# Kernel tuning notes

Hardware: AMD Instinct MI355X
Metric: run time of the kernel (lower is better)

The kernel has to match this reference:

```python
import jax, jax.numpy as jnp
import numpy as np

EPS_NORM = 1e-7
EPS_FLOW = 1e-8
GAMMA = 5.0
ETA = 1.0
NU = 1.0
SIGMA = 0.1
TAU_FLOW, TAU_COLOR, TAU_PROX = 0.8, 0.7, 0.5
SAM_TEMP = 1.0  # sam_weight used as temperature


def _cdist(x):
    # x: [B,N,D] -> pairwise euclidean distances [B,N,N]
    sq = jnp.sum(x * x, axis=-1)
    d2 = sq[..., :, None] + sq[..., None, :] - 2.0 * jnp.einsum('bnd,bmd->bnm', x, x)
    return jnp.sqrt(jnp.maximum(d2, 0.0))


def _within_sample_loss(features, sim_scores, tau, mask):
    # features: [B,N,D] (raw), sim_scores: [B,N,N], mask: [B,N] float
    nf = features / (jnp.linalg.norm(features, axis=-1, keepdims=True) + EPS_NORM)
    g_plus = jax.nn.sigmoid(-GAMMA * (tau - sim_scores))   # 1/(1+exp(gamma*(tau-s)))
    g_minus = jax.nn.sigmoid(-GAMMA * (sim_scores - tau))  # 1/(1+exp(gamma*(s-tau)))
    fs = jnp.einsum('bnd,bmd->bnm', nf, nf)
    s_plus_exp = jnp.sum(jnp.exp(ETA * fs * g_plus), axis=-1)   # [B,N]
    s_minus_exp = jnp.sum(jnp.exp(-NU * fs * g_minus), axis=-1)
    loss_per_point = jnp.log1p(s_plus_exp) / ETA + jnp.log1p(s_minus_exp) / NU
    loss_per_point = loss_per_point * mask
    valid_points = jnp.sum(mask, axis=-1)
    loss = jnp.mean(jnp.sum(loss_per_point, axis=-1) / valid_points)
    return -loss


def _sam_loss(features, labels):
    # masked_contrastive_loss with temperature = sam_weight
    nf = features / (jnp.linalg.norm(features, axis=-1, keepdims=True) + EPS_NORM)
    logits = jnp.einsum('bnd,bmd->bnm', nf, nf) / SAM_TEMP
    pos = (labels[:, :, None] == labels[:, None, :]).astype(logits.dtype)
    neg = 1.0 - pos
    exp_logits = jnp.exp(logits)
    denom = exp_logits + jnp.sum(exp_logits * neg, axis=2, keepdims=True)
    neg_log_likelihood = -jnp.log(exp_logits / denom)
    w = pos / jnp.maximum(jnp.sum(pos, axis=2, keepdims=True), 1e-6)
    nll = jnp.sum(neg_log_likelihood * w, axis=2)  # [B,N]
    pos_sum = jnp.sum(pos, axis=2)
    valid = 1.0 - (pos_sum == 0).astype(logits.dtype)
    w2 = valid / jnp.maximum(jnp.sum(valid, axis=1, keepdims=True), 1e-6)
    return jnp.mean(jnp.sum(nll * w2, axis=1))


def _forward(features, flow, points, colors_f, mask_f, sam):
    m_outer = mask_f[:, :, None] * mask_f[:, None, :]
    # flow cosine similarity
    fn = jnp.linalg.norm(flow, axis=-1)
    flow_sim = jnp.einsum('bnd,bmd->bnm', flow, flow) / (fn[:, :, None] * fn[:, None, :] + EPS_FLOW)
    flow_sim = flow_sim * m_outer
    # color similarity: 1 - normalized euclidean distance of RGB/255
    c = colors_f / 255.0
    color_sim = (1.0 - _cdist(c) / jnp.sqrt(jnp.asarray(c.shape[-1], c.dtype))) * m_outer
    # proximity similarity
    prox_sim = jnp.exp(-_cdist(points) / (2.0 * SIGMA ** 2)) * m_outer

    flow_loss = _within_sample_loss(features, flow_sim, TAU_FLOW, mask_f)
    color_loss = _within_sample_loss(features, color_sim, TAU_COLOR, mask_f)
    prox_loss = _within_sample_loss(features, prox_sim, TAU_PROX, mask_f)
    sam_loss = _sam_loss(features, sam)
    return 1.0 * flow_loss + 1.0 * color_loss + 1.0 * prox_loss + 1.0 * sam_loss


def setup_inputs() -> dict:
    key = jax.random.key(0)
    k1, k2, k3, k4, k5 = jax.random.split(key, 5)
    B, N, D = 4, 2048, 64
    features = jax.random.normal(k1, (B, N, D), dtype=jnp.float32)
    flow = jax.random.normal(k2, (B, N, 3), dtype=jnp.float32)
    points = jax.random.uniform(k3, (B, N, 3), dtype=jnp.float32)
    colors = jax.random.randint(k4, (B, N, 3), 0, 256, dtype=jnp.int32)
    sam = jax.random.randint(k5, (B, N), 0, 64, dtype=jnp.int32)
    mask = jnp.ones((B, N), dtype=bool)
    return {"features": features, "flow": flow, "points": points,
            "colors": colors, "sam": sam, "mask": mask}


def reference(features, flow, points, colors, sam, mask):
    mask_f = mask.astype(features.dtype)
    colors_f = colors.astype(features.dtype)
    return _forward(features, flow, points, colors_f, mask_f, sam)
```

## Files before the change

kernel.cpp:

```cpp
#include <hip/hip_runtime.h>

typedef unsigned short ushort_t;
typedef unsigned int uint_t;
typedef __attribute__((ext_vector_type(8))) short short8;
typedef __attribute__((ext_vector_type(4))) float float4v;

#define NPTS 2048
#define DIM 64
#define BATCH 4
#define CH 16
#define MC 128
#define NFS 72

__device__ inline float fexp2(float x){ return __builtin_amdgcn_exp2f(x); }
__device__ inline float frcp(float x){ return __builtin_amdgcn_rcpf(x); }
__device__ inline float fsqrt_(float x){ return __builtin_amdgcn_sqrtf(x); }

__device__ inline ushort_t f2bf(float x){
    uint_t u = __float_as_uint(x);
    u += 0x7FFF + ((u >> 16) & 1);
    return (ushort_t)(u >> 16);
}

__global__ __launch_bounds__(256) void fpc_prep(
    const float* __restrict__ feat, const float* __restrict__ flow,
    const float* __restrict__ pts, const int* __restrict__ cols,
    ushort_t* __restrict__ nf_g, float* __restrict__ aux_g)
{
    int t = blockIdx.x * 256 + threadIdx.x;
    const float4* f4 = (const float4*)(feat + (size_t)t * DIM);
    float v[DIM];
    float ss = 0.f;
#pragma unroll
    for (int i = 0; i < 16; i++){
        float4 x = f4[i];
        v[4*i+0] = x.x; v[4*i+1] = x.y; v[4*i+2] = x.z; v[4*i+3] = x.w;
        ss += x.x*x.x + x.y*x.y + x.z*x.z + x.w*x.w;
    }
    float inv = frcp(fsqrt_(ss) + 1e-7f);
    uint_t* np_ = (uint_t*)(nf_g + (size_t)t * DIM);
#pragma unroll
    for (int i = 0; i < 32; i++){
        uint_t lo = f2bf(v[2*i] * inv), hi = f2bf(v[2*i+1] * inv);
        np_[i] = lo | (hi << 16);
    }
    float fx = flow[t*3+0], fy = flow[t*3+1], fz = flow[t*3+2];
    float fa = fsqrt_(fx*fx + fy*fy + fz*fz);
    float* a = aux_g + (size_t)t * 10;
    a[0]=fx; a[1]=fy; a[2]=fz; a[3]=fa;
    a[4]=pts[t*3+0]; a[5]=pts[t*3+1]; a[6]=pts[t*3+2];
    const float s255 = 1.0f/255.0f;
    a[7]=(float)cols[t*3+0]*s255; a[8]=(float)cols[t*3+1]*s255; a[9]=(float)cols[t*3+2]*s255;
}

__global__ __launch_bounds__(256) void fpc_main(
    const ushort_t* __restrict__ nf_g, const float* __restrict__ aux_g,
    const int* __restrict__ lab_g, float* __restrict__ part)
{
    __shared__ __align__(16) ushort_t lds_nf[MC * NFS];
    __shared__ float lds_aux[MC * 10];
    __shared__ int lds_lab[MC];

    const int tid = threadIdx.x;
    const int ch = blockIdx.x, rg = blockIdx.y, b = blockIdx.z;
    const int mbase = ch * MC;
    const int bpt = b * NPTS;

#pragma unroll
    for (int i = 0; i < 4; i++){
        int cid = tid + i * 256;
        int row = cid >> 3, sub = cid & 7;
        const uint4* src = (const uint4*)(nf_g + (size_t)(bpt + mbase + row) * DIM + sub * 8);
        *(uint4*)(&lds_nf[row * NFS + sub * 8]) = *src;
    }
    {
        const float* asrc = aux_g + (size_t)(bpt + mbase) * 10;
#pragma unroll
        for (int i = 0; i < 5; i++){ int w = tid + i * 256; lds_aux[w] = asrc[w]; }
        if (tid < MC) lds_lab[tid] = lab_g[bpt + mbase + tid];
    }
    __syncthreads();

    const int lane = tid & 63, wave = tid >> 6;
    const int q = lane >> 4, c = lane & 15;
    const int rowA = rg * 64 + wave * 16;

    const ushort_t* arow = nf_g + (size_t)(bpt + rowA + c) * DIM;
    short8 a0 = *(const short8*)(arow + q * 8);
    short8 a1 = *(const short8*)(arow + 32 + q * 8);

    float rf[4][10]; int rlab[4];
#pragma unroll
    for (int r = 0; r < 4; r++){
        int n = bpt + rowA + q * 4 + r;
        const float* a = aux_g + (size_t)n * 10;
#pragma unroll
        for (int k = 0; k < 10; k++) rf[r][k] = a[k];
        rlab[r] = lab_g[n];
    }

    float acc[4][10];
#pragma unroll
    for (int r = 0; r < 4; r++)
#pragma unroll
        for (int k = 0; k < 10; k++) acc[r][k] = 0.0f;

    const float L2E  = 1.4426950408889634f;
    const float GL2E = 7.213475204444817f;
    const float CF = GL2E * 0.8f, CC = GL2E * 0.7f, CP = GL2E * 0.5f;

    for (int mt = 0; mt < MC / 16; mt++){
        int mloc = mt * 16 + c;
        const ushort_t* brow = &lds_nf[mloc * NFS];
        short8 b0 = *(const short8*)(brow + q * 8);
        short8 b1 = *(const short8*)(brow + 32 + q * 8);
        float4v fs4 = {0.f, 0.f, 0.f, 0.f};
        fs4 = __builtin_amdgcn_mfma_f32_16x16x32_bf16(a0, b0, fs4, 0, 0, 0);
        fs4 = __builtin_amdgcn_mfma_f32_16x16x32_bf16(a1, b1, fs4, 0, 0, 0);

        const float* ma = &lds_aux[mloc * 10];
        float m0=ma[0], m1=ma[1], m2=ma[2], m3=ma[3], m4=ma[4];
        float m5=ma[5], m6=ma[6], m7=ma[7], m8=ma[8], m9=ma[9];
        int mlab = lds_lab[mloc];

#pragma unroll
        for (int r = 0; r < 4; r++){
            float fs = fs4[r];
            float efs = L2E * fs;
            float dotf = rf[r][0]*m0 + rf[r][1]*m1 + rf[r][2]*m2;
            float sflow = dotf * frcp(rf[r][3]*m3 + 1e-8f);
            {
                float u  = fexp2(CF - GL2E * sflow);
                float gp = frcp(1.0f + u);
                float gm = 1.0f - gp;
                acc[r][0] += fexp2(efs * gp);
                acc[r][1] += fexp2(-efs * gm);
            }
            float dx = rf[r][7]-m7, dy = rf[r][8]-m8, dz = rf[r][9]-m9;
            float scol = 1.0f - fsqrt_(dx*dx + dy*dy + dz*dz) * 0.5773502691896258f;
            {
                float u  = fexp2(CC - GL2E * scol);
                float gp = frcp(1.0f + u);
                float gm = 1.0f - gp;
                acc[r][2] += fexp2(efs * gp);
                acc[r][3] += fexp2(-efs * gm);
            }
            float px = rf[r][4]-m4, py = rf[r][5]-m5, pz = rf[r][6]-m6;
            float dpt = fsqrt_(px*px + py*py + pz*pz);
            float sprox = fexp2(dpt * -72.13475204444817f);
            {
                float u  = fexp2(CP - GL2E * sprox);
                float gp = frcp(1.0f + u);
                float gm = 1.0f - gp;
                acc[r][4] += fexp2(efs * gp);
                acc[r][5] += fexp2(-efs * gm);
            }
            float e = fexp2(efs);
            acc[r][6] += e;
            bool pos = (rlab[r] == mlab);
            acc[r][7] += pos ? e : 0.0f;
            acc[r][8] += pos ? fs : 0.0f;
            acc[r][9] += pos ? 1.0f : 0.0f;
        }
    }

#pragma unroll
    for (int r = 0; r < 4; r++)
#pragma unroll
        for (int k = 0; k < 10; k++){
            float v = acc[r][k];
            v += __shfl_xor(v, 1, 64);
            v += __shfl_xor(v, 2, 64);
            v += __shfl_xor(v, 4, 64);
            v += __shfl_xor(v, 8, 64);
            acc[r][k] = v;
        }
    if (c == 0){
#pragma unroll
        for (int r = 0; r < 4; r++){
            int n = rowA + q * 4 + r;
            size_t base = ((size_t)(b * CH + ch) * 10) * NPTS + n;
#pragma unroll
            for (int k = 0; k < 10; k++) part[base + (size_t)k * NPTS] = acc[r][k];
        }
    }
}

__global__ __launch_bounds__(256) void fpc_final(
    const float* __restrict__ part, float* __restrict__ out)
{
    int t = blockIdx.x * 256 + threadIdx.x;
    int b = t >> 11, n = t & (NPTS - 1);
    float S[10];
#pragma unroll
    for (int k = 0; k < 10; k++){
        float s = 0.f;
        for (int ch2 = 0; ch2 < CH; ch2++)
            s += part[((size_t)(b * CH + ch2) * 10 + k) * NPTS + n];
        S[k] = s;
    }
    float lpp = log1pf(S[0]) + log1pf(S[1]) + log1pf(S[2])
              + log1pf(S[3]) + log1pf(S[4]) + log1pf(S[5]);
    float Sneg = S[6] - S[7];
    float ipc  = 1.0f / S[9];
    float sam = logf(Sneg) + (S[7] / Sneg - S[8]) * ipc;
    float val = (sam - lpp) * (1.0f / (BATCH * (float)NPTS));

    __shared__ float red[256];
    red[threadIdx.x] = val;
    __syncthreads();
    for (int s = 128; s > 0; s >>= 1){
        if (threadIdx.x < s) red[threadIdx.x] += red[threadIdx.x + s];
        __syncthreads();
    }
    if (threadIdx.x == 0) atomicAdd(out, red[0]);
}

extern "C" void kernel_launch(void* const* d_in, const int* in_sizes, int n_in,
                              void* d_out, int out_size, void* d_ws, size_t ws_size,
                              hipStream_t stream)
{
    const float* feat = (const float*)d_in[0];
    const float* flow = (const float*)d_in[1];
    const float* pts  = (const float*)d_in[2];
    const int*   cols = (const int*)d_in[3];
    const int*   sam  = (const int*)d_in[4];

    char* ws = (char*)d_ws;
    ushort_t* nf_g  = (ushort_t*)ws;
    float*    aux_g = (float*)(ws + (1u << 20));
    float*    part  = (float*)(ws + (1u << 20) + (512u << 10));

    hipMemsetAsync(d_out, 0, sizeof(float), stream);
    hipLaunchKernelGGL(fpc_prep, dim3(32), dim3(256), 0, stream,
                       feat, flow, pts, cols, nf_g, aux_g);
    hipLaunchKernelGGL(fpc_main, dim3(CH, 32, BATCH), dim3(256), 0, stream,
                       nf_g, aux_g, sam, part);
    hipLaunchKernelGGL(fpc_final, dim3(32), dim3(256), 0, stream, part, (float*)d_out);
}
```

Baseline: 128.8 us.

## Simplify gate math, pack aux data, halve column chunks, atomically accumulate partials

```diff
diff --git a/kernel.cpp b/kernel.cpp
--- a/kernel.cpp
+++ b/kernel.cpp
@@ -8,9 +8,10 @@
 #define NPTS 2048
 #define DIM 64
 #define BATCH 4
-#define CH 16
+#define CH 8
 #define MC 128
 #define NFS 72
+#define AUXS 12
 
 __device__ inline float fexp2(float x){ return __builtin_amdgcn_exp2f(x); }
 __device__ inline float frcp(float x){ return __builtin_amdgcn_rcpf(x); }
@@ -25,62 +26,56 @@
 __global__ __launch_bounds__(256) void fpc_prep(
     const float* __restrict__ feat, const float* __restrict__ flow,
     const float* __restrict__ pts, const int* __restrict__ cols,
+    const int* __restrict__ lab,
     ushort_t* __restrict__ nf_g, float* __restrict__ aux_g)
 {
-    int t = blockIdx.x * 256 + threadIdx.x;
-    const float4* f4 = (const float4*)(feat + (size_t)t * DIM);
-    float v[DIM];
-    float ss = 0.f;
-#pragma unroll
-    for (int i = 0; i < 16; i++){
-        float4 x = f4[i];
-        v[4*i+0] = x.x; v[4*i+1] = x.y; v[4*i+2] = x.z; v[4*i+3] = x.w;
-        ss += x.x*x.x + x.y*x.y + x.z*x.z + x.w*x.w;
-    }
+    int gid = blockIdx.x * 256 + threadIdx.x;
+    int t = gid >> 2, sub = gid & 3;
+    const float4* f4 = (const float4*)(feat + (size_t)t * DIM + sub * 16);
+    float4 x0 = f4[0], x1 = f4[1], x2 = f4[2], x3 = f4[3];
+    float ss = x0.x*x0.x + x0.y*x0.y + x0.z*x0.z + x0.w*x0.w
+             + x1.x*x1.x + x1.y*x1.y + x1.z*x1.z + x1.w*x1.w
+             + x2.x*x2.x + x2.y*x2.y + x2.z*x2.z + x2.w*x2.w
+             + x3.x*x3.x + x3.y*x3.y + x3.z*x3.z + x3.w*x3.w;
+    ss += __shfl_xor(ss, 1, 64);
+    ss += __shfl_xor(ss, 2, 64);
     float inv = frcp(fsqrt_(ss) + 1e-7f);
-    uint_t* np_ = (uint_t*)(nf_g + (size_t)t * DIM);
-#pragma unroll
-    for (int i = 0; i < 32; i++){
+
+    float v[16] = {x0.x,x0.y,x0.z,x0.w, x1.x,x1.y,x1.z,x1.w,
+                   x2.x,x2.y,x2.z,x2.w, x3.x,x3.y,x3.z,x3.w};
+    uint_t w8[8];
+#pragma unroll
+    for (int i = 0; i < 8; i++){
         uint_t lo = f2bf(v[2*i] * inv), hi = f2bf(v[2*i+1] * inv);
-        np_[i] = lo | (hi << 16);
-    }
-    float fx = flow[t*3+0], fy = flow[t*3+1], fz = flow[t*3+2];
-    float fa = fsqrt_(fx*fx + fy*fy + fz*fz);
-    float* a = aux_g + (size_t)t * 10;
-    a[0]=fx; a[1]=fy; a[2]=fz; a[3]=fa;
-    a[4]=pts[t*3+0]; a[5]=pts[t*3+1]; a[6]=pts[t*3+2];
-    const float s255 = 1.0f/255.0f;
-    a[7]=(float)cols[t*3+0]*s255; a[8]=(float)cols[t*3+1]*s255; a[9]=(float)cols[t*3+2]*s255;
-}
-
-__global__ __launch_bounds__(256) void fpc_main(
+        w8[i] = lo | (hi << 16);
+    }
+    uint4* dst = (uint4*)(nf_g + (size_t)t * DIM + sub * 16);
+    dst[0] = make_uint4(w8[0], w8[1], w8[2], w8[3]);
+    dst[1] = make_uint4(w8[4], w8[5], w8[6], w8[7]);
+
+    if (sub == 0){
+        float fx = flow[t*3+0], fy = flow[t*3+1], fz = flow[t*3+2];
+        float fi = frcp(fsqrt_(fx*fx + fy*fy + fz*fz) + 1e-8f);
+        const float s255 = 1.0f/255.0f;
+        float4 a0 = make_float4(fx*fi, fy*fi, fz*fi, pts[t*3+0]);
+        float4 a1 = make_float4(pts[t*3+1], pts[t*3+2],
+                                (float)cols[t*3+0]*s255, (float)cols[t*3+1]*s255);
+        float4 a2 = make_float4((float)cols[t*3+2]*s255, (float)lab[t], 0.f, 0.f);
+        float4* ad = (float4*)(aux_g + (size_t)t * AUXS);
+        ad[0] = a0; ad[1] = a1; ad[2] = a2;
+    }
+}
+
+__global__ __launch_bounds__(256, 4) void fpc_main(
     const ushort_t* __restrict__ nf_g, const float* __restrict__ aux_g,
-    const int* __restrict__ lab_g, float* __restrict__ part)
+    float* __restrict__ part2)
 {
     __shared__ __align__(16) ushort_t lds_nf[MC * NFS];
-    __shared__ float lds_aux[MC * 10];
-    __shared__ int lds_lab[MC];
+    __shared__ __align__(16) float lds_aux[MC * AUXS];
 
     const int tid = threadIdx.x;
     const int ch = blockIdx.x, rg = blockIdx.y, b = blockIdx.z;
-    const int mbase = ch * MC;
     const int bpt = b * NPTS;
-
-#pragma unroll
-    for (int i = 0; i < 4; i++){
-        int cid = tid + i * 256;
-        int row = cid >> 3, sub = cid & 7;
-        const uint4* src = (const uint4*)(nf_g + (size_t)(bpt + mbase + row) * DIM + sub * 8);
-        *(uint4*)(&lds_nf[row * NFS + sub * 8]) = *src;
-    }
-    {
-        const float* asrc = aux_g + (size_t)(bpt + mbase) * 10;
-#pragma unroll
-        for (int i = 0; i < 5; i++){ int w = tid + i * 256; lds_aux[w] = asrc[w]; }
-        if (tid < MC) lds_lab[tid] = lab_g[bpt + mbase + tid];
-    }
-    __syncthreads();
-
     const int lane = tid & 63, wave = tid >> 6;
     const int q = lane >> 4, c = lane & 15;
     const int rowA = rg * 64 + wave * 16;
@@ -89,14 +84,15 @@
     short8 a0 = *(const short8*)(arow + q * 8);
     short8 a1 = *(const short8*)(arow + 32 + q * 8);
 
-    float rf[4][10]; int rlab[4];
+    float rf[4][9]; float rlabf[4];
 #pragma unroll
     for (int r = 0; r < 4; r++){
-        int n = bpt + rowA + q * 4 + r;
-        const float* a = aux_g + (size_t)n * 10;
-#pragma unroll
-        for (int k = 0; k < 10; k++) rf[r][k] = a[k];
-        rlab[r] = lab_g[n];
+        const float4* ap = (const float4*)(aux_g + (size_t)(bpt + rowA + q*4 + r) * AUXS);
+        float4 v0 = ap[0], v1 = ap[1], v2 = ap[2];
+        rf[r][0]=v0.x; rf[r][1]=v0.y; rf[r][2]=v0.z;
+        rf[r][3]=v0.w; rf[r][4]=v1.x; rf[r][5]=v1.y;
+        rf[r][6]=v1.z; rf[r][7]=v1.w; rf[r][8]=v2.x;
+        rlabf[r]=v2.y;
     }
 
     float acc[4][10];
@@ -107,60 +103,68 @@
 
     const float L2E  = 1.4426950408889634f;
     const float GL2E = 7.213475204444817f;
-    const float CF = GL2E * 0.8f, CC = GL2E * 0.7f, CP = GL2E * 0.5f;
-
-    for (int mt = 0; mt < MC / 16; mt++){
-        int mloc = mt * 16 + c;
-        const ushort_t* brow = &lds_nf[mloc * NFS];
-        short8 b0 = *(const short8*)(brow + q * 8);
-        short8 b1 = *(const short8*)(brow + 32 + q * 8);
-        float4v fs4 = {0.f, 0.f, 0.f, 0.f};
-        fs4 = __builtin_amdgcn_mfma_f32_16x16x32_bf16(a0, b0, fs4, 0, 0, 0);
-        fs4 = __builtin_amdgcn_mfma_f32_16x16x32_bf16(a1, b1, fs4, 0, 0, 0);
-
-        const float* ma = &lds_aux[mloc * 10];
-        float m0=ma[0], m1=ma[1], m2=ma[2], m3=ma[3], m4=ma[4];
-        float m5=ma[5], m6=ma[6], m7=ma[7], m8=ma[8], m9=ma[9];
-        int mlab = lds_lab[mloc];
-
-#pragma unroll
-        for (int r = 0; r < 4; r++){
-            float fs = fs4[r];
-            float efs = L2E * fs;
-            float dotf = rf[r][0]*m0 + rf[r][1]*m1 + rf[r][2]*m2;
-            float sflow = dotf * frcp(rf[r][3]*m3 + 1e-8f);
-            {
-                float u  = fexp2(CF - GL2E * sflow);
-                float gp = frcp(1.0f + u);
-                float gm = 1.0f - gp;
-                acc[r][0] += fexp2(efs * gp);
-                acc[r][1] += fexp2(-efs * gm);
+
+    for (int cpass = 0; cpass < 2; cpass++){
+        if (cpass) __syncthreads();
+        const int mbase = (ch * 2 + cpass) * MC;
+#pragma unroll
+        for (int i = 0; i < 4; i++){
+            int cid = tid + i * 256;
+            int row = cid >> 3, s8 = cid & 7;
+            *(uint4*)(&lds_nf[row * NFS + s8 * 8]) =
+                *(const uint4*)(nf_g + (size_t)(bpt + mbase + row) * DIM + s8 * 8);
+        }
+        {
+            const float4* asrc = (const float4*)(aux_g + (size_t)(bpt + mbase) * AUXS);
+            float4* adst = (float4*)lds_aux;
+            adst[tid] = asrc[tid];
+            if (tid < 128) adst[256 + tid] = asrc[256 + tid];
+        }
+        __syncthreads();
+
+        for (int mt = 0; mt < MC / 16; mt++){
+            int mloc = mt * 16 + c;
+            const ushort_t* brow = &lds_nf[mloc * NFS];
+            short8 b0 = *(const short8*)(brow + q * 8);
+            short8 b1 = *(const short8*)(brow + 32 + q * 8);
+            float4v fs4 = {0.f, 0.f, 0.f, 0.f};
+            fs4 = __builtin_amdgcn_mfma_f32_16x16x32_bf16(a0, b0, fs4, 0, 0, 0);
+            fs4 = __builtin_amdgcn_mfma_f32_16x16x32_bf16(a1, b1, fs4, 0, 0, 0);
+
+            const float4* ma4 = (const float4*)(&lds_aux[mloc * AUXS]);
+            float4 m0v = ma4[0], m1v = ma4[1], m2v = ma4[2];
+            float mu0=m0v.x, mu1=m0v.y, mu2=m0v.z;
+            float mp0=m0v.w, mp1=m1v.x, mp2=m1v.y;
+            float mc0=m1v.z, mc1=m1v.w, mc2=m2v.x;
+            float mlabf=m2v.y;
+
+#pragma unroll
+            for (int r = 0; r < 4; r++){
+                float fs  = fs4[r];
+                float efs = L2E * fs;
+                float e   = fexp2(efs);
+                float emi = frcp(e);
+                float sflow = rf[r][0]*mu0 + rf[r][1]*mu1 + rf[r][2]*mu2;
+                float uf = fexp2(fmaf(sflow, -GL2E, 5.770780163555854f));
+                float tf = fexp2(efs * frcp(1.0f + uf));
+                acc[r][0] += tf; acc[r][1] = fmaf(emi, tf, acc[r][1]);
+                float dx = rf[r][6]-mc0, dy = rf[r][7]-mc1, dz = rf[r][8]-mc2;
+                float sq = fsqrt_(dx*dx + dy*dy + dz*dz);
+                float uc = fexp2(fmaf(sq, 4.1647034f, -2.1640425613334451f));
+                float tc = fexp2(efs * frcp(1.0f + uc));
+                acc[r][2] += tc; acc[r][3] = fmaf(emi, tc, acc[r][3]);
+                float px = rf[r][3]-mp0, py = rf[r][4]-mp1, pz = rf[r][5]-mp2;
+                float dp = fsqrt_(px*px + py*py + pz*pz);
+                float sp = fexp2(-72.13475204444817f * dp);
+                float up = fexp2(fmaf(sp, -GL2E, 3.6067376022224085f));
+                float tp = fexp2(efs * frcp(1.0f + up));
+                acc[r][4] += tp; acc[r][5] = fmaf(emi, tp, acc[r][5]);
+                float pm = (rlabf[r] == mlabf) ? 1.0f : 0.0f;
+                acc[r][6] += e;
+                acc[r][7] = fmaf(pm, e,  acc[r][7]);
+                acc[r][8] = fmaf(pm, fs, acc[r][8]);
+                acc[r][9] += pm;
             }
-            float dx = rf[r][7]-m7, dy = rf[r][8]-m8, dz = rf[r][9]-m9;
-            float scol = 1.0f - fsqrt_(dx*dx + dy*dy + dz*dz) * 0.5773502691896258f;
-            {
-                float u  = fexp2(CC - GL2E * scol);
-                float gp = frcp(1.0f + u);
-                float gm = 1.0f - gp;
-                acc[r][2] += fexp2(efs * gp);
-                acc[r][3] += fexp2(-efs * gm);
-            }
-            float px = rf[r][4]-m4, py = rf[r][5]-m5, pz = rf[r][6]-m6;
-            float dpt = fsqrt_(px*px + py*py + pz*pz);
-            float sprox = fexp2(dpt * -72.13475204444817f);
-            {
-                float u  = fexp2(CP - GL2E * sprox);
-                float gp = frcp(1.0f + u);
-                float gm = 1.0f - gp;
-                acc[r][4] += fexp2(efs * gp);
-                acc[r][5] += fexp2(-efs * gm);
-            }
-            float e = fexp2(efs);
-            acc[r][6] += e;
-            bool pos = (rlab[r] == mlab);
-            acc[r][7] += pos ? e : 0.0f;
-            acc[r][8] += pos ? fs : 0.0f;
-            acc[r][9] += pos ? 1.0f : 0.0f;
         }
     }
 
@@ -178,32 +182,23 @@
     if (c == 0){
 #pragma unroll
         for (int r = 0; r < 4; r++){
-            int n = rowA + q * 4 + r;
-            size_t base = ((size_t)(b * CH + ch) * 10) * NPTS + n;
-#pragma unroll
-            for (int k = 0; k < 10; k++) part[base + (size_t)k * NPTS] = acc[r][k];
+            float* dst = part2 + (size_t)(bpt + rowA + q*4 + r) * AUXS;
+#pragma unroll
+            for (int k = 0; k < 10; k++) atomicAdd(dst + k, acc[r][k]);
         }
     }
 }
 
 __global__ __launch_bounds__(256) void fpc_final(
-    const float* __restrict__ part, float* __restrict__ out)
+    const float* __restrict__ part2, float* __restrict__ out)
 {
     int t = blockIdx.x * 256 + threadIdx.x;
-    int b = t >> 11, n = t & (NPTS - 1);
-    float S[10];
-#pragma unroll
-    for (int k = 0; k < 10; k++){
-        float s = 0.f;
-        for (int ch2 = 0; ch2 < CH; ch2++)
-            s += part[((size_t)(b * CH + ch2) * 10 + k) * NPTS + n];
-        S[k] = s;
-    }
-    float lpp = log1pf(S[0]) + log1pf(S[1]) + log1pf(S[2])
-              + log1pf(S[3]) + log1pf(S[4]) + log1pf(S[5]);
-    float Sneg = S[6] - S[7];
-    float ipc  = 1.0f / S[9];
-    float sam = logf(Sneg) + (S[7] / Sneg - S[8]) * ipc;
+    const float4* p = (const float4*)(part2 + (size_t)t * AUXS);
+    float4 v0 = p[0], v1 = p[1], v2 = p[2];
+    float lpp = log1pf(v0.x) + log1pf(v0.y) + log1pf(v0.z)
+              + log1pf(v0.w) + log1pf(v1.x) + log1pf(v1.y);
+    float Sneg = v1.z - v1.w;
+    float sam = logf(Sneg) + (v1.w / Sneg - v2.x) / v2.y;
     float val = (sam - lpp) * (1.0f / (BATCH * (float)NPTS));
 
     __shared__ float red[256];
@@ -229,12 +224,13 @@
     char* ws = (char*)d_ws;
     ushort_t* nf_g  = (ushort_t*)ws;
     float*    aux_g = (float*)(ws + (1u << 20));
-    float*    part  = (float*)(ws + (1u << 20) + (512u << 10));
-
+    float*    part2 = (float*)(ws + (1u << 20) + 393216u);
+
+    hipMemsetAsync(part2, 0, BATCH * NPTS * AUXS * sizeof(float), stream);
     hipMemsetAsync(d_out, 0, sizeof(float), stream);
-    hipLaunchKernelGGL(fpc_prep, dim3(32), dim3(256), 0, stream,
-                       feat, flow, pts, cols, nf_g, aux_g);
+    hipLaunchKernelGGL(fpc_prep, dim3(128), dim3(256), 0, stream,
+                       feat, flow, pts, cols, sam, nf_g, aux_g);
     hipLaunchKernelGGL(fpc_main, dim3(CH, 32, BATCH), dim3(256), 0, stream,
-                       nf_g, aux_g, sam, part);
-    hipLaunchKernelGGL(fpc_final, dim3(32), dim3(256), 0, stream, part, (float*)d_out);
-}
+                       nf_g, aux_g, part2);
+    hipLaunchKernelGGL(fpc_final, dim3(32), dim3(256), 0, stream, part2, (float*)d_out);
+}
```

Measured after the change: 329.3 us. 156% more time.
